# Kernel optimization log

Measured on AMD Instinct MI355X. Metric: run time of the kernel, lower is better.

The kernel has to match this reference:

```python
import jax, jax.numpy as jnp
import numpy as np

B, L, D = 2, 1024, 768
N_LAYERS, D_STATE, D_CONV, EXPAND = 4, 16, 4, 2
D_INNER = EXPAND * D
DT_RANK = (D + 15) // 16  # 48, ceil(d_model/16) as in reference Mamba
N_CLS = 10
EPS = 1e-6


def rmsnorm(x, w):
    return x * jax.lax.rsqrt(jnp.mean(x * x, axis=-1, keepdims=True) + EPS) * w


def mamba_block(x, in_w, conv_w, conv_b, xp_w, dt_w, dt_b, A_log, D_skip, out_w):
    # x: (B, L, D)
    Bsz = x.shape[0]
    xz = jnp.einsum('bld,ed->ble', x, in_w)            # (B, L, 2*d_inner)
    xi, z = jnp.split(xz, 2, axis=-1)
    # causal depthwise conv over the sequence dim
    xc = jnp.transpose(xi, (0, 2, 1))                  # (B, d_inner, L)
    xc = jax.lax.conv_general_dilated(
        xc, conv_w[:, None, :], (1,), [(D_CONV - 1, 0)],
        dimension_numbers=('NCH', 'OIH', 'NCH'), feature_group_count=D_INNER)
    xc = jnp.transpose(xc, (0, 2, 1)) + conv_b         # (B, L, d_inner)
    xc = jax.nn.silu(xc)
    # input-dependent SSM parameters
    x_dbl = jnp.einsum('bld,ed->ble', xc, xp_w)        # (B, L, dt_rank + 2*d_state)
    dt, Bs, Cs = jnp.split(x_dbl, [DT_RANK, DT_RANK + D_STATE], axis=-1)
    delta = jax.nn.softplus(jnp.einsum('blr,dr->bld', dt, dt_w) + dt_b)  # (B, L, d_inner)
    A = -jnp.exp(A_log)                                # (d_inner, d_state)
    dA = jnp.exp(delta[..., None] * A)                 # (B, L, d_inner, d_state)
    dBu = delta[..., None] * Bs[:, :, None, :] * xc[..., None]

    def step(h, inp):
        dA_t, dBu_t, C_t = inp
        h = dA_t * h + dBu_t                           # (B, d_inner, d_state)
        y = jnp.einsum('bdn,bn->bd', h, C_t)
        return h, y

    h0 = jnp.zeros((Bsz, D_INNER, D_STATE), x.dtype)
    _, ys = jax.lax.scan(step, h0, (jnp.swapaxes(dA, 0, 1),
                                    jnp.swapaxes(dBu, 0, 1),
                                    jnp.swapaxes(Cs, 0, 1)))
    y = jnp.swapaxes(ys, 0, 1) + xc * D_skip           # (B, L, d_inner)
    y = y * jax.nn.silu(z)                             # gate
    return jnp.einsum('bld,od->blo', y, out_w)


def reference(x, norm_w, in_proj_w, conv_w, conv_b, x_proj_w, dt_proj_w, dt_proj_b,
              A_log, D_skip, out_proj_w, final_norm_w,
              head1_w, head1_b, head_norm_w, head2_w, head2_b):
    for i in range(N_LAYERS):
        res = x
        x = rmsnorm(x, norm_w[i])
        x = mamba_block(x, in_proj_w[i], conv_w[i], conv_b[i], x_proj_w[i],
                        dt_proj_w[i], dt_proj_b[i], A_log[i], D_skip[i],
                        out_proj_w[i]) + res
    x = rmsnorm(x, final_norm_w)
    last = x[:, -1, :]                                 # (B, D)
    h = last @ head1_w.T + head1_b
    h = rmsnorm(h, head_norm_w)
    h = jax.nn.gelu(h, approximate=False)              # torch nn.GELU default is exact erf
    return h @ head2_w.T + head2_b                     # (B, N_CLS)


def setup_inputs() -> dict:
    key = jax.random.key(0)
    ks = jax.random.split(key, 10)
    s = 0.02
    x = jax.random.normal(ks[0], (B, L, D), jnp.float32)
    norm_w = jnp.ones((N_LAYERS, D), jnp.float32)
    in_proj_w = s * jax.random.normal(ks[1], (N_LAYERS, 2 * D_INNER, D), jnp.float32)
    conv_w = s * jax.random.normal(ks[2], (N_LAYERS, D_INNER, D_CONV), jnp.float32)
    conv_b = jnp.zeros((N_LAYERS, D_INNER), jnp.float32)
    x_proj_w = s * jax.random.normal(ks[3], (N_LAYERS, DT_RANK + 2 * D_STATE, D_INNER), jnp.float32)
    dt_proj_w = s * jax.random.normal(ks[4], (N_LAYERS, D_INNER, DT_RANK), jnp.float32)
    dt_proj_b = jnp.full((N_LAYERS, D_INNER), -4.6, jnp.float32)  # softplus(-4.6) ~ 0.01
    A_log = jnp.log(jnp.broadcast_to(
        jnp.arange(1, D_STATE + 1, dtype=jnp.float32), (N_LAYERS, D_INNER, D_STATE)) + 0.0)
    D_skip = jnp.ones((N_LAYERS, D_INNER), jnp.float32)
    out_proj_w = s * jax.random.normal(ks[5], (N_LAYERS, D, D_INNER), jnp.float32)
    final_norm_w = jnp.ones((D,), jnp.float32)
    head1_w = s * jax.random.normal(ks[6], (D, D), jnp.float32)
    head1_b = jnp.zeros((D,), jnp.float32)
    head_norm_w = jnp.ones((D,), jnp.float32)
    head2_w = s * jax.random.normal(ks[7], (N_CLS, D), jnp.float32)
    head2_b = jnp.zeros((N_CLS,), jnp.float32)
    return {"x": x, "norm_w": norm_w, "in_proj_w": in_proj_w, "conv_w": conv_w,
            "conv_b": conv_b, "x_proj_w": x_proj_w, "dt_proj_w": dt_proj_w,
            "dt_proj_b": dt_proj_b, "A_log": A_log, "D_skip": D_skip,
            "out_proj_w": out_proj_w, "final_norm_w": final_norm_w,
            "head1_w": head1_w, "head1_b": head1_b, "head_norm_w": head_norm_w,
            "head2_w": head2_w, "head2_b": head2_b}
```

## Files before the change

kernel.cpp:

```cpp
#include <hip/hip_runtime.h>
#include <hip/hip_bf16.h>
#include <math.h>

typedef __bf16 bf16;
typedef __bf16 bf16x4 __attribute__((ext_vector_type(4)));
typedef __bf16 bf16x8 __attribute__((ext_vector_type(8)));
typedef float floatx4 __attribute__((ext_vector_type(4)));

#define BB 2
#define LL 1024
#define DD 768
#define DI 1536
#define MROWS 2048
#define NXP 80
#define DTRANK 48
#define DTPAD 64
#define DSTATE 16
#define NC 16
#define CLEN 64
#define KSPLIT 16
#define OPKS 4
#define LOG2E 1.4426950408889634f
#define TROW 132
#define SYROW 68

__device__ __forceinline__ void ld16(void* lds, const void* g) {
    __builtin_amdgcn_global_load_lds(
        (const __attribute__((address_space(1))) void*)g,
        (__attribute__((address_space(3))) void*)lds, 16, 0, 0);
}

__device__ __forceinline__ void wait_vm0() {
    asm volatile("s_waitcnt vmcnt(0)" ::: "memory");
}

__device__ __forceinline__ float row16_sum(float x) {
    float t;
    t = __int_as_float(__builtin_amdgcn_update_dpp(0, __float_as_int(x), 0x111, 0xF, 0xF, true)); x += t;
    t = __int_as_float(__builtin_amdgcn_update_dpp(0, __float_as_int(x), 0x112, 0xF, 0xF, true)); x += t;
    t = __int_as_float(__builtin_amdgcn_update_dpp(0, __float_as_int(x), 0x114, 0xF, 0xF, true)); x += t;
    t = __int_as_float(__builtin_amdgcn_update_dpp(0, __float_as_int(x), 0x118, 0xF, 0xF, true)); x += t;
    return x;
}

__device__ __forceinline__ float exp2_raw(float x) {
#if __has_builtin(__builtin_amdgcn_exp2f)
    return __builtin_amdgcn_exp2f(x);
#else
    float r; asm("v_exp_f32 %0, %1" : "=v"(r) : "v"(x)); return r;
#endif
}

#define N1 (4 * 3072 * 768)
#define N2 (4 * NXP * DI)
#define N3 (4 * DI * DTPAD)
#define N4 (4 * DD * DI)
__global__ __launch_bounds__(256) void cvt_all_k(const float* __restrict__ in_proj_w,
                                                 const float* __restrict__ x_proj_w,
                                                 const float* __restrict__ dt_proj_w,
                                                 const float* __restrict__ out_proj_w,
                                                 bf16* __restrict__ w_in,
                                                 bf16* __restrict__ w_xp,
                                                 bf16* __restrict__ w_dt,
                                                 bf16* __restrict__ w_out) {
    int i = blockIdx.x * 256 + threadIdx.x;
    if (i < N1) { w_in[i] = (bf16)in_proj_w[i]; return; }
    i -= N1;
    if (i < N2) { w_xp[i] = (bf16)x_proj_w[i]; return; }
    i -= N2;
    if (i < N3) {
        int row = i >> 6, c = i & 63;
        w_dt[i] = (c < DTRANK) ? (bf16)dt_proj_w[row * DTRANK + c] : (bf16)0.f;
        return;
    }
    i -= N3;
    if (i < N4) w_out[i] = (bf16)out_proj_w[i];
}

__global__ __launch_bounds__(256) void rmsnorm_k(const float* __restrict__ x,
                                                 const float* __restrict__ w,
                                                 bf16* __restrict__ out) {
    int row = blockIdx.x;
    const float* xr = x + (size_t)row * DD;
    int tid = threadIdx.x;
    float v[3]; float ss = 0.f;
    for (int j = 0; j < 3; j++) { v[j] = xr[tid + j * 256]; ss += v[j] * v[j]; }
    for (int o = 1; o < 64; o <<= 1) ss += __shfl_xor(ss, o, 64);
    __shared__ float sred[4];
    if ((tid & 63) == 0) sred[tid >> 6] = ss;
    __syncthreads();
    float scale = rsqrtf((sred[0] + sred[1] + sred[2] + sred[3]) / (float)DD + 1e-6f);
    for (int j = 0; j < 3; j++) {
        int c = tid + j * 256;
        out[(size_t)row * DD + c] = (bf16)(v[j] * scale * w[c]);
    }
}

template <int MODE>
__global__ __launch_bounds__(256) void gemm_bt(const bf16* __restrict__ A,
                                               const bf16* __restrict__ W,
                                               float* __restrict__ Cf,
                                               bf16* __restrict__ Cb,
                                               int M, int N, int K) {
    __shared__ bf16 As[128][32];
    __shared__ bf16 Ws[128][32];
    const int tid  = threadIdx.x;
    const int m0   = blockIdx.x * 128;
    const int n0   = blockIdx.y * 128;
    const int wave = tid >> 6;
    const int lane = tid & 63;
    const int wm   = (wave >> 1) * 64;
    const int wn   = (wave & 1) * 64;
    const int lrow = lane & 15;
    const int quad = lane >> 4;

    int kbeg = 0, kend = K;
    if constexpr (MODE == 5) {
        int kseg = K / gridDim.z;
        kbeg = blockIdx.z * kseg;
        kend = kbeg + kseg;
        Cf  += (size_t)blockIdx.z * M * N;
    }

    floatx4 acc[4][4];
    for (int mi = 0; mi < 4; mi++)
        for (int ni = 0; ni < 4; ni++) acc[mi][ni] = (floatx4){0.f, 0.f, 0.f, 0.f};

    const int r0  = tid >> 2;
    const int r1  = r0 + 64;
    const int seg = (tid & 3) * 8;
    char* asb0 = (char*)As + wave * 1024;
    char* asb1 = (char*)As + 4096 + wave * 1024;
    char* wsb0 = (char*)Ws + wave * 1024;
    char* wsb1 = (char*)Ws + 4096 + wave * 1024;

    for (int kb = kbeg; kb < kend; kb += 32) {
        int gk = kb + seg;
        __syncthreads();
        ld16(asb0, A + (size_t)(m0 + r0) * K + gk);
        ld16(asb1, A + (size_t)(m0 + r1) * K + gk);
        ld16(wsb0, W + (size_t)(n0 + r0) * K + gk);
        ld16(wsb1, W + (size_t)(n0 + r1) * K + gk);
        wait_vm0();
        __syncthreads();
        bf16x8 af[4], wf[4];
        for (int mi = 0; mi < 4; mi++) af[mi] = *(const bf16x8*)&As[wm + mi * 16 + lrow][quad * 8];
        for (int ni = 0; ni < 4; ni++) wf[ni] = *(const bf16x8*)&Ws[wn + ni * 16 + lrow][quad * 8];
        for (int mi = 0; mi < 4; mi++)
            for (int ni = 0; ni < 4; ni++)
                acc[mi][ni] = __builtin_amdgcn_mfma_f32_16x16x32_bf16(af[mi], wf[ni], acc[mi][ni], 0, 0, 0);
    }
    for (int mi = 0; mi < 4; mi++) {
        int rowb = m0 + wm + mi * 16 + quad * 4;
        for (int ni = 0; ni < 4; ni++) {
            int col = n0 + wn + ni * 16 + lrow;
            for (int r = 0; r < 4; r++) {
                int row = rowb + r;
                float v = acc[mi][ni][r];
                if constexpr (MODE == 1) Cb[(size_t)row * N + col] = (bf16)v;
                else                     Cf[(size_t)row * N + col] = v;
            }
        }
    }
}

__global__ __launch_bounds__(256) void op_reduce_norm_k(const float* __restrict__ part,
                                                        const float* __restrict__ resid,
                                                        const float* __restrict__ nw,
                                                        float* __restrict__ xout,
                                                        bf16* __restrict__ xnb) {
    int row = blockIdx.x;
    int tid = threadIdx.x;
    float v[3]; float ss = 0.f;
    for (int j = 0; j < 3; j++) {
        int c = tid + j * 256;
        size_t idx = (size_t)row * DD + c;
        float s = resid[idx];
        for (int ks = 0; ks < OPKS; ks++) s += part[(size_t)ks * MROWS * DD + idx];
        v[j] = s;
        xout[idx] = s;
        ss += s * s;
    }
    for (int o = 1; o < 64; o <<= 1) ss += __shfl_xor(ss, o, 64);
    __shared__ float sred[4];
    if ((tid & 63) == 0) sred[tid >> 6] = ss;
    __syncthreads();
    float scale = rsqrtf((sred[0] + sred[1] + sred[2] + sred[3]) / (float)DD + 1e-6f);
    for (int j = 0; j < 3; j++) {
        int c = tid + j * 256;
        xnb[(size_t)row * DD + c] = (bf16)(v[j] * scale * nw[c]);
    }
}

__global__ __launch_bounds__(256) void gemm_xp(const bf16* __restrict__ A,
                                               const bf16* __restrict__ W,
                                               float* __restrict__ part) {
    __shared__ bf16 As[64][40];
    __shared__ bf16 Ws[128][40];
    const int tid  = threadIdx.x;
    const int m0   = blockIdx.x * 64;
    const int ks   = blockIdx.y;
    const int k0   = ks * (DI / KSPLIT);
    const int wave = tid >> 6;
    const int lane = tid & 63;
    const int lrow = lane & 15;
    const int quad = lane >> 4;
    const int wm   = wave * 16;

    floatx4 acc[5];
    for (int ni = 0; ni < 5; ni++) acc[ni] = (floatx4){0.f, 0.f, 0.f, 0.f};

    const int ra  = tid >> 2;
    const int rw1 = ra + 64;
    const int seg = (tid & 3) * 8;

    for (int kb = 0; kb < DI / KSPLIT; kb += 32) {
        int gk = k0 + kb + seg;
        bf16x8 va = *(const bf16x8*)(A + (size_t)(m0 + ra) * DI + gk);
        bf16x8 vw0, vw1;
        if (ra < NXP) vw0 = *(const bf16x8*)(W + (size_t)ra * DI + gk);
        else          for (int j = 0; j < 8; j++) vw0[j] = (bf16)0.f;
        if (rw1 < NXP) vw1 = *(const bf16x8*)(W + (size_t)rw1 * DI + gk);
        else           for (int j = 0; j < 8; j++) vw1[j] = (bf16)0.f;
        __syncthreads();
        *(bf16x8*)&As[ra][seg]  = va;
        *(bf16x8*)&Ws[ra][seg]  = vw0;
        *(bf16x8*)&Ws[rw1][seg] = vw1;
        __syncthreads();
        bf16x8 af = *(const bf16x8*)&As[wm + lrow][quad * 8];
        for (int ni = 0; ni < 5; ni++) {
            bf16x8 wf = *(const bf16x8*)&Ws[ni * 16 + lrow][quad * 8];
            acc[ni] = __builtin_amdgcn_mfma_f32_16x16x32_bf16(af, wf, acc[ni], 0, 0, 0);
        }
    }
    float* pout = part + (size_t)ks * MROWS * NXP;
    for (int ni = 0; ni < 5; ni++) {
        int col = ni * 16 + lrow;
        for (int r = 0; r < 4; r++) {
            int row = m0 + wm + quad * 4 + r;
            pout[(size_t)row * NXP + col] = acc[ni][r];
        }
    }
}

__global__ __launch_bounds__(256) void xp_reduce_k(const float* __restrict__ part,
                                                   float* __restrict__ xdbl,
                                                   bf16* __restrict__ dtbf) {
    int idx = blockIdx.x * 256 + threadIdx.x;
    if (idx >= MROWS * NXP) return;
    float s = 0.f;
    for (int j = 0; j < KSPLIT; j++) s += part[(size_t)j * MROWS * NXP + idx];
    xdbl[idx] = s;
    int m = idx / NXP, c = idx - m * NXP;
    if (c < DTRANK)      dtbf[m * DTPAD + c] = (bf16)s;
    else if (c < DTPAD)  dtbf[m * DTPAD + c] = (bf16)0.f;
}

__global__ __launch_bounds__(256) void conv_silu_k(const bf16* __restrict__ xz,
                                                   const float* __restrict__ cw,
                                                   const float* __restrict__ cb,
                                                   bf16* __restrict__ xcb,
                                                   bf16* __restrict__ gzb) {
    int t = blockIdx.x * 256 + threadIdx.x;
    if (t >= MROWS * (DI / 4)) return;
    int m = t / (DI / 4);
    int d = (t - m * (DI / 4)) * 4;
    int l = m & (LL - 1);
    float acc[4];
    floatx4 cwv[4];
    for (int q = 0; q < 4; q++) {
        acc[q] = cb[d + q];
        cwv[q] = *(const floatx4*)&cw[(d + q) * 4];
    }
    for (int k = 0; k < 4; k++) {
        int lp = l - 3 + k;
        if (lp >= 0) {
            bf16x4 v = *(const bf16x4*)&xz[(size_t)(m - 3 + k) * (2 * DI) + d];
            for (int q = 0; q < 4; q++) acc[q] += (float)v[q] * cwv[q][k];
        }
    }
    bf16x4 xo, go;
    bf16x4 z4 = *(const bf16x4*)&xz[(size_t)m * (2 * DI) + DI + d];
    for (int q = 0; q < 4; q++) {
        float s = acc[q] / (1.f + __expf(-acc[q]));
        xo[q] = (bf16)s;
        float zv = (float)z4[q];
        go[q] = (bf16)(zv / (1.f + __expf(-zv)));
    }
    *(bf16x4*)&xcb[(size_t)m * DI + d] = xo;
    *(bf16x4*)&gzb[(size_t)m * DI + d] = go;
}

__global__ __launch_bounds__(256) void scan1_k(const bf16* __restrict__ dtb,
                                               const bf16* __restrict__ wdt,
                                               const float* __restrict__ dtbias,
                                               const bf16* __restrict__ xcb,
                                               const float* __restrict__ xdbl,
                                               const float* __restrict__ A_log,
                                               float* __restrict__ Pbuf,
                                               float* __restrict__ Sbuf) {
    const int b   = blockIdx.y;
    const int d0  = blockIdx.x * 16;
    const int c   = blockIdx.z;
    const int tid = threadIdx.x;
    const int dl  = tid >> 4;
    const int n   = tid & 15;
    const int wv  = tid >> 6;
    const int lane = tid & 63;
    const int lr  = lane & 15;
    const int q   = lane >> 4;
    const int l0  = c * CLEN;

    const float a2 = -__expf(A_log[(size_t)(d0 + dl) * DSTATE + n]) * LOG2E;
    const float bi = dtbias[d0 + lr];

    __shared__ __align__(16) bf16  Bdt[16][72];
    __shared__ __align__(16) bf16  Adt[CLEN][64];
    __shared__ __align__(16) float sbraw[CLEN][16];
    __shared__ __align__(16) bf16  sxc[CLEN][16];
    __shared__ __align__(16) float sdpT[16][TROW];
    __shared__ __align__(16) float sbT[16][68];

    {
        int s = tid, row = s >> 3, cc = s & 7;
        ld16((char*)&Adt[0][0] + (s & ~63) * 16,
             dtb + (size_t)(b * LL + l0 + row) * DTPAD + ((cc ^ (row & 7)) << 3));
        s = tid + 256; row = s >> 3; cc = s & 7;
        ld16((char*)&Adt[0][0] + (s & ~63) * 16,
             dtb + (size_t)(b * LL + l0 + row) * DTPAD + ((cc ^ (row & 7)) << 3));
        {
            int r2 = tid >> 2, c2 = tid & 3;
            ld16((char*)&sbraw[0][0] + (tid & ~63) * 16,
                 xdbl + (size_t)(b * LL + l0 + r2) * NXP + DTRANK + c2 * 4);
        }
        if (tid < 128) {
            int r2 = tid >> 1, c2 = tid & 1;
            ld16((char*)&sxc[0][0] + (tid & ~63) * 16,
                 xcb + (size_t)(b * LL + l0 + r2) * DI + d0 + c2 * 8);
            int r = tid >> 3, s2 = (tid & 7) * 8;
            *(bf16x8*)&Bdt[r][s2] = *(const bf16x8*)&wdt[(size_t)(d0 + r) * DTPAD + s2];
        }
    }
    wait_vm0();
    __syncthreads();

    {
        floatx4 dacc = (floatx4){0.f, 0.f, 0.f, 0.f};
        const char* arow = (const char*)&Adt[16 * wv + lr][0];
        bf16x8 a0 = *(const bf16x8*)(arow + ((q ^ (lr & 7)) << 4));
        bf16x8 a1 = *(const bf16x8*)(arow + (((4 + q) ^ (lr & 7)) << 4));
        dacc = __builtin_amdgcn_mfma_f32_16x16x32_bf16(
            a0, *(const bf16x8*)&Bdt[lr][q * 8], dacc, 0, 0, 0);
        dacc = __builtin_amdgcn_mfma_f32_16x16x32_bf16(
            a1, *(const bf16x8*)&Bdt[lr][32 + q * 8], dacc, 0, 0, 0);
        float vv[4], xvv[4];
        #pragma unroll
        for (int r = 0; r < 4; ++r) {
            int l = 16 * wv + q * 4 + r;
            float v = dacc[r] + bi;
            v = (v > 20.f) ? v : log1pf(__expf(v));
            vv[r] = v; xvv[r] = (float)sxc[l][lr];
        }
        int L0 = 16 * wv + q * 4;
        *(float4*)&sdpT[lr][2 * L0] =
            make_float4(vv[0], vv[0] * xvv[0], vv[1], vv[1] * xvv[1]);
        *(float4*)&sdpT[lr][2 * L0 + 4] =
            make_float4(vv[2], vv[2] * xvv[2], vv[3], vv[3] * xvv[3]);
        #pragma unroll
        for (int k2 = 0; k2 < 4; ++k2) {
            int idx = tid + 256 * k2, ii = idx >> 4, dd2 = idx & 15;
            sbT[dd2][ii] = sbraw[ii][dd2];
        }
    }
    __syncthreads();

    float h = 0.f, sd = 0.f;
    {
        const float4* dpr = (const float4*)&sdpT[dl][0];
        const float4* bpr = (const float4*)&sbT[n][0];
        float4 dA[4], dB2[4], bA[2], bB2[2];
        #pragma unroll
        for (int t = 0; t < 4; ++t) dA[t] = dpr[t];
        #pragma unroll
        for (int t = 0; t < 2; ++t) bA[t] = bpr[t];
        #pragma unroll
        for (int g = 0; g < 8; ++g) {
            if (g + 1 < 8) {
                #pragma unroll
                for (int t = 0; t < 4; ++t) {
                    if ((g & 1) == 0) dB2[t] = dpr[(g + 1) * 4 + t];
                    else              dA[t]  = dpr[(g + 1) * 4 + t];
                }
                #pragma unroll
                for (int t = 0; t < 2; ++t) {
                    if ((g & 1) == 0) bB2[t] = bpr[(g + 1) * 2 + t];
                    else              bA[t]  = bpr[(g + 1) * 2 + t];
                }
            }
            #pragma unroll
            for (int i = 0; i < 8; ++i) {
                float4 v = ((g & 1) == 0) ? dA[i >> 1] : dB2[i >> 1];
                float4 w = ((g & 1) == 0) ? bA[i >> 2] : bB2[i >> 2];
                float dvx = (i & 1) ? v.z : v.x;
                float dpy = (i & 1) ? v.w : v.y;
                float bx  = ((i & 3) == 0) ? w.x : ((i & 3) == 1) ? w.y
                          : ((i & 3) == 2) ? w.z : w.w;
                float e = exp2_raw(dvx * a2);
                h = __builtin_fmaf(e, h, dpy * bx);
                sd += dvx;
            }
        }
    }
    size_t o = (((size_t)c * BB + b) * DI + (d0 + dl)) * DSTATE + n;
    Pbuf[o] = exp2_raw(a2 * sd);
    Sbuf[o] = h;
}

__global__ __launch_bounds__(256) void compose_k(const float* __restrict__ P,
                                                 const float* __restrict__ S,
                                                 float* __restrict__ H0) {
    int idx = blockIdx.x * 256 + threadIdx.x;
    const size_t stride = (size_t)BB * DI * DSTATE;
    float h = 0.f;
    #pragma unroll
    for (int c = 0; c < NC; ++c) {
        H0[(size_t)c * stride + idx] = h;
        h = __builtin_fmaf(P[(size_t)c * stride + idx], h, S[(size_t)c * stride + idx]);
    }
}

__global__ __launch_bounds__(256) void scan2_k(const bf16* __restrict__ dtb,
                                               const bf16* __restrict__ wdt,
                                               const float* __restrict__ dtbias,
                                               const bf16* __restrict__ xcb,
                                               const bf16* __restrict__ gzb,
                                               const float* __restrict__ xdbl,
                                               const float* __restrict__ A_log,
                                               const float* __restrict__ Dskip,
                                               const float* __restrict__ H0buf,
                                               bf16* __restrict__ ybf) {
    const int b   = blockIdx.y;
    const int d0  = blockIdx.x * 16;
    const int c   = blockIdx.z;
    const int tid = threadIdx.x;
    const int dl  = tid >> 4;
    const int n   = tid & 15;
    const int wv  = tid >> 6;
    const int lane = tid & 63;
    const int lr  = lane & 15;
    const int q   = lane >> 4;
    const int l0  = c * CLEN;

    const float a2 = -__expf(A_log[(size_t)(d0 + dl) * DSTATE + n]) * LOG2E;
    const float bi = dtbias[d0 + lr];

    __shared__ __align__(16) bf16  Bdt[16][72];
    __shared__ __align__(16) bf16  sxc[CLEN][16];
    __shared__ __align__(16) bf16  sgz[CLEN][16];
    __shared__ __align__(16) float sdpT[16][TROW];
    __shared__ __align__(16) float sbcT[16][TROW];
    __shared__ __align__(16) char  sov[16384];
    bf16  (*Adt)[64]     = (bf16 (*)[64])sov;
    float (*sbcraw)[32]  = (float (*)[32])(sov + 8192);
    float (*syT)[SYROW]  = (float (*)[SYROW])sov;

    float h = H0buf[((size_t)c * BB + b) * (DI * DSTATE) + (size_t)(d0 + dl) * DSTATE + n];

    {
        int s = tid, row = s >> 3, cc = s & 7;
        ld16((char*)&Adt[0][0] + (s & ~63) * 16,
             dtb + (size_t)(b * LL + l0 + row) * DTPAD + ((cc ^ (row & 7)) << 3));
        ld16((char*)&sbcraw[0][0] + (s & ~63) * 16,
             xdbl + (size_t)(b * LL + l0 + row) * NXP + DTRANK + cc * 4);
        s = tid + 256; row = s >> 3; cc = s & 7;
        ld16((char*)&Adt[0][0] + (s & ~63) * 16,
             dtb + (size_t)(b * LL + l0 + row) * DTPAD + ((cc ^ (row & 7)) << 3));
        ld16((char*)&sbcraw[0][0] + (s & ~63) * 16,
             xdbl + (size_t)(b * LL + l0 + row) * NXP + DTRANK + cc * 4);
        if (tid < 128) {
            int r2 = tid >> 1, c2 = tid & 1;
            ld16((char*)&sxc[0][0] + (tid & ~63) * 16,
                 xcb + (size_t)(b * LL + l0 + r2) * DI + d0 + c2 * 8);
            int r = tid >> 3, s2 = (tid & 7) * 8;
            *(bf16x8*)&Bdt[r][s2] = *(const bf16x8*)&wdt[(size_t)(d0 + r) * DTPAD + s2];
        } else {
            int t2 = tid - 128, r2 = t2 >> 1, c2 = t2 & 1;
            ld16((char*)&sgz[0][0] + (t2 & ~63) * 16,
                 gzb + (size_t)(b * LL + l0 + r2) * DI + d0 + c2 * 8);
        }
    }
    wait_vm0();
    __syncthreads();

    {
        floatx4 dacc = (floatx4){0.f, 0.f, 0.f, 0.f};
        const char* arow = (const char*)&Adt[16 * wv + lr][0];
        bf16x8 a0 = *(const bf16x8*)(arow + ((q ^ (lr & 7)) << 4));
        bf16x8 a1 = *(const bf16x8*)(arow + (((4 + q) ^ (lr & 7)) << 4));
        dacc = __builtin_amdgcn_mfma_f32_16x16x32_bf16(
            a0, *(const bf16x8*)&Bdt[lr][q * 8], dacc, 0, 0, 0);
        dacc = __builtin_amdgcn_mfma_f32_16x16x32_bf16(
            a1, *(const bf16x8*)&Bdt[lr][32 + q * 8], dacc, 0, 0, 0);
        float vv[4], xvv[4];
        #pragma unroll
        for (int r = 0; r < 4; ++r) {
            int l = 16 * wv + q * 4 + r;
            float v = dacc[r] + bi;
            v = (v > 20.f) ? v : log1pf(__expf(v));
            vv[r] = v; xvv[r] = (float)sxc[l][lr];
        }
        int L0 = 16 * wv + q * 4;
        *(float4*)&sdpT[lr][2 * L0] =
            make_float4(vv[0], vv[0] * xvv[0], vv[1], vv[1] * xvv[1]);
        *(float4*)&sdpT[lr][2 * L0 + 4] =
            make_float4(vv[2], vv[2] * xvv[2], vv[3], vv[3] * xvv[3]);
        #pragma unroll
        for (int k2 = 0; k2 < 4; ++k2) {
            int idx = tid + 256 * k2, ii = idx >> 4, dd2 = idx & 15;
            *(float2*)&sbcT[dd2][2 * ii] =
                make_float2(sbcraw[ii][dd2], sbcraw[ii][16 + dd2]);
        }
    }
    __syncthreads();

    {
        const float4* dpr = (const float4*)&sdpT[dl][0];
        const float4* bcr = (const float4*)&sbcT[n][0];
        float4 dA[4], bA[4], dB2[4], bB2[4];
        float y4[4];
        #pragma unroll
        for (int t = 0; t < 4; ++t) { dA[t] = dpr[t]; bA[t] = bcr[t]; }
        #pragma unroll
        for (int g = 0; g < 8; ++g) {
            #pragma unroll
            for (int t = 0; t < 4; ++t) {
                if (g + 1 < 8) {
                    if ((g & 1) == 0) { dB2[t] = dpr[(g + 1) * 4 + t]; bB2[t] = bcr[(g + 1) * 4 + t]; }
                    else              { dA[t]  = dpr[(g + 1) * 4 + t]; bA[t]  = bcr[(g + 1) * 4 + t]; }
                }
            }
            #pragma unroll
            for (int i = 0; i < 8; ++i) {
                float4 v = ((g & 1) == 0) ? dA[i >> 1] : dB2[i >> 1];
                float4 w = ((g & 1) == 0) ? bA[i >> 1] : bB2[i >> 1];
                float dvx = (i & 1) ? v.z : v.x;
                float dpy = (i & 1) ? v.w : v.y;
                float bx  = (i & 1) ? w.z : w.x;
                float cy  = (i & 1) ? w.w : w.y;
                float e = exp2_raw(dvx * a2);
                h = __builtin_fmaf(e, h, dpy * bx);
                y4[i & 3] = row16_sum(h * cy);
                if ((i & 3) == 3 && n == 0) {
                    *(floatx4*)&syT[dl][g * 8 + i - 3] =
                        (floatx4){y4[0], y4[1], y4[2], y4[3]};
                }
            }
        }
    }
    __syncthreads();

    #pragma unroll
    for (int k2 = 0; k2 < 4; ++k2) {
        int idx = tid + 256 * k2, ii = idx >> 4, dd = idx & 15;
        float xv = (float)sxc[ii][dd];
        float gv = (float)sgz[ii][dd];
        float yv = (syT[dd][ii] + xv * Dskip[d0 + dd]) * gv;
        ybf[(size_t)(b * LL + l0 + ii) * DI + d0 + dd] = (bf16)yv;
    }
}

__global__ __launch_bounds__(256) void head_norm_k(const float* __restrict__ x,
                                                   const float* __restrict__ fnw,
                                                   float* __restrict__ xn_buf) {
    int b = blockIdx.x;
    int tid = threadIdx.x;
    const float* xr = x + ((size_t)b * LL + (LL - 1)) * DD;
    __shared__ float sred[4];
    float v[3]; float ss = 0.f;
    for (int j = 0; j < 3; j++) { v[j] = xr[tid + j * 256]; ss += v[j] * v[j]; }
    for (int o = 1; o < 64; o <<= 1) ss += __shfl_xor(ss, o, 64);
    if ((tid & 63) == 0) sred[tid >> 6] = ss;
    __syncthreads();
    float scale = rsqrtf((sred[0] + sred[1] + sred[2] + sred[3]) / (float)DD + 1e-6f);
    for (int j = 0; j < 3; j++) {
        int c = tid + j * 256;
        xn_buf[(size_t)b * DD + c] = v[j] * scale * fnw[c];
    }
}

__global__ __launch_bounds__(256) void head_h1_k(const float* __restrict__ xn_buf,
                                                 const float* __restrict__ h1w,
                                                 const float* __restrict__ h1b,
                                                 float* __restrict__ h_buf) {
    int b  = blockIdx.x;
    int o0 = blockIdx.y * 64;
    int tid = threadIdx.x;
    __shared__ float sx[DD];
    for (int c = tid; c < DD; c += 256) sx[c] = xn_buf[(size_t)b * DD + c];
    __syncthreads();
    int wave = tid >> 6, lane = tid & 63;
    for (int j = 0; j < 16; j++) {
        int o = o0 + wave * 16 + j;
        const float* wrow = h1w + (size_t)o * DD;
        float acc = 0.f;
        for (int k = 0; k < 12; k++) {
            int c = lane + 64 * k;
            acc += wrow[c] * sx[c];
        }
        for (int off = 1; off < 64; off <<= 1) acc += __shfl_xor(acc, off, 64);
        if (lane == 0) h_buf[(size_t)b * DD + o] = acc + h1b[o];
    }
}

__global__ __launch_bounds__(256) void head_out_k(const float* __restrict__ h_buf,
                                                  const float* __restrict__ hnw,
                                                  const float* __restrict__ h2w,
                                                  const float* __restrict__ h2b,
                                                  float* __restrict__ out) {
    int b = blockIdx.x;
    int tid = threadIdx.x;
    __shared__ float hh[DD];
    __shared__ float sred[4];
    const float* hr = h_buf + (size_t)b * DD;
    float ss = 0.f;
    for (int c = tid; c < DD; c += 256) { float v = hr[c]; ss += v * v; }
    for (int o = 1; o < 64; o <<= 1) ss += __shfl_xor(ss, o, 64);
    if ((tid & 63) == 0) sred[tid >> 6] = ss;
    __syncthreads();
    float sc = rsqrtf((sred[0] + sred[1] + sred[2] + sred[3]) / (float)DD + 1e-6f);
    for (int c = tid; c < DD; c += 256) {
        float v = hr[c] * sc * hnw[c];
        hh[c] = 0.5f * v * (1.f + erff(v * 0.70710678118f));
    }
    __syncthreads();
    int w = tid >> 6, lane = tid & 63;
    for (int j = w; j < 10; j += 4) {
        float acc = 0.f;
        const float* wrow = h2w + (size_t)j * DD;
        for (int c = lane; c < DD; c += 64) acc += hh[c] * wrow[c];
        for (int o = 1; o < 64; o <<= 1) acc += __shfl_xor(acc, o, 64);
        if (lane == 0) out[b * 10 + j] = acc + h2b[j];
    }
}

extern "C" void kernel_launch(void* const* d_in, const int* in_sizes, int n_in,
                              void* d_out, int out_size, void* d_ws, size_t ws_size,
                              hipStream_t stream) {
    const float* x_in      = (const float*)d_in[0];
    const float* norm_w    = (const float*)d_in[1];
    const float* in_proj_w = (const float*)d_in[2];
    const float* conv_w    = (const float*)d_in[3];
    const float* conv_b    = (const float*)d_in[4];
    const float* x_proj_w  = (const float*)d_in[5];
    const float* dt_proj_w = (const float*)d_in[6];
    const float* dt_proj_b = (const float*)d_in[7];
    const float* A_log     = (const float*)d_in[8];
    const float* D_skip    = (const float*)d_in[9];
    const float* out_proj_w= (const float*)d_in[10];
    const float* fnw       = (const float*)d_in[11];
    const float* h1w       = (const float*)d_in[12];
    const float* h1b       = (const float*)d_in[13];
    const float* hnw       = (const float*)d_in[14];
    const float* h2w       = (const float*)d_in[15];
    const float* h2b       = (const float*)d_in[16];
    float* out = (float*)d_out;

    char* ws = (char*)d_ws;
    size_t off = 0;
    auto alloc = [&](size_t bytes) -> void* {
        void* p = ws + off;
        off += (bytes + 255) & ~(size_t)255;
        return p;
    };
    bf16* w_in  = (bf16*)alloc((size_t)N1 * 2);
    bf16* w_xp  = (bf16*)alloc((size_t)N2 * 2);
    bf16* w_dt  = (bf16*)alloc((size_t)N3 * 2);
    bf16* w_out = (bf16*)alloc((size_t)N4 * 2);
    bf16* xn_bf = (bf16*)alloc((size_t)MROWS * DD * 2);
    bf16* xz_bf = (bf16*)alloc((size_t)MROWS * 2 * DI * 2);
    bf16* xc_bf = (bf16*)alloc((size_t)MROWS * DI * 2);
    bf16* gz_bf = (bf16*)alloc((size_t)MROWS * DI * 2);
    float* xdbl = (float*)alloc((size_t)MROWS * NXP * 4);
    bf16* dt_bf = (bf16*)alloc((size_t)MROWS * DTPAD * 2);
    bf16* y_bf  = (bf16*)alloc((size_t)MROWS * DI * 2);
    float* x_buf= (float*)alloc((size_t)MROWS * DD * 4);
    float* Pbuf = (float*)alloc((size_t)NC * BB * DI * DSTATE * 4);
    float* Sbuf = (float*)alloc((size_t)NC * BB * DI * DSTATE * 4);
    float* H0buf= (float*)alloc((size_t)NC * BB * DI * DSTATE * 4);
    float* xnl  = (float*)alloc((size_t)BB * DD * 4);
    float* hbuf = (float*)alloc((size_t)BB * DD * 4);
    float* xp_part = (float*)alloc((size_t)KSPLIT * MROWS * NXP * 4);
    float* op_part = (float*)alloc((size_t)OPKS * MROWS * DD * 4);

    {
        int ntot = N1 + N2 + N3 + N4;
        cvt_all_k<<<(ntot + 255) / 256, 256, 0, stream>>>(
            in_proj_w, x_proj_w, dt_proj_w, out_proj_w, w_in, w_xp, w_dt, w_out);
    }

    for (int i = 0; i < 4; i++) {
        const float* x_src = (i == 0) ? x_in : x_buf;
        if (i == 0)
            rmsnorm_k<<<MROWS, 256, 0, stream>>>(x_src, norm_w, xn_bf);
        gemm_bt<1><<<dim3(MROWS / 128, 3072 / 128), 256, 0, stream>>>(
            xn_bf, w_in + (size_t)i * 3072 * 768, nullptr, xz_bf,
            MROWS, 2 * DI, DD);
        conv_silu_k<<<(MROWS * (DI / 4) + 255) / 256, 256, 0, stream>>>(
            xz_bf, conv_w + (size_t)i * DI * 4, conv_b + (size_t)i * DI, xc_bf, gz_bf);
        gemm_xp<<<dim3(MROWS / 64, KSPLIT), 256, 0, stream>>>(
            xc_bf, w_xp + (size_t)i * NXP * DI, xp_part);
        xp_reduce_k<<<(MROWS * NXP + 255) / 256, 256, 0, stream>>>(xp_part, xdbl, dt_bf);
        scan1_k<<<dim3(DI / 16, BB, NC), 256, 0, stream>>>(
            dt_bf, w_dt + (size_t)i * DI * DTPAD, dt_proj_b + (size_t)i * DI,
            xc_bf, xdbl, A_log + (size_t)i * DI * DSTATE, Pbuf, Sbuf);
        compose_k<<<(BB * DI * DSTATE) / 256, 256, 0, stream>>>(Pbuf, Sbuf, H0buf);
        scan2_k<<<dim3(DI / 16, BB, NC), 256, 0, stream>>>(
            dt_bf, w_dt + (size_t)i * DI * DTPAD, dt_proj_b + (size_t)i * DI,
            xc_bf, gz_bf, xdbl, A_log + (size_t)i * DI * DSTATE,
            D_skip + (size_t)i * DI, H0buf, y_bf);
        gemm_bt<5><<<dim3(MROWS / 128, DD / 128, OPKS), 256, 0, stream>>>(
            y_bf, w_out + (size_t)i * DD * DI, op_part, nullptr,
            MROWS, DD, DI);
        op_reduce_norm_k<<<MROWS, 256, 0, stream>>>(
            op_part, x_src, norm_w + ((i + 1) & 3) * DD, x_buf, xn_bf);
    }

    head_norm_k<<<BB, 256, 0, stream>>>(x_buf, fnw, xnl);
    head_h1_k<<<dim3(BB, DD / 64), 256, 0, stream>>>(xnl, h1w, h1b, hbuf);
    head_out_k<<<BB, 256, 0, stream>>>(hbuf, hnw, h2w, h2b, out);
}
```

Baseline: 658.5 us.

## Process two chunks per scan block with register prefetch of next chunk

```diff
diff --git a/kernel.cpp b/kernel.cpp
--- a/kernel.cpp
+++ b/kernel.cpp
@@ -301,7 +301,7 @@
                                                float* __restrict__ Sbuf) {
     const int b   = blockIdx.y;
     const int d0  = blockIdx.x * 16;
-    const int c   = blockIdx.z;
+    const int c0  = blockIdx.z * 2;
     const int tid = threadIdx.x;
     const int dl  = tid >> 4;
     const int n   = tid & 15;
@@ -309,50 +309,40 @@
     const int lane = tid & 63;
     const int lr  = lane & 15;
     const int q   = lane >> 4;
-    const int l0  = c * CLEN;
 
     const float a2 = -__expf(A_log[(size_t)(d0 + dl) * DSTATE + n]) * LOG2E;
     const float bi = dtbias[d0 + lr];
 
-    __shared__ __align__(16) bf16  Bdt[16][72];
-    __shared__ __align__(16) bf16  Adt[CLEN][64];
-    __shared__ __align__(16) float sbraw[CLEN][16];
     __shared__ __align__(16) bf16  sxc[CLEN][16];
     __shared__ __align__(16) float sdpT[16][TROW];
     __shared__ __align__(16) float sbT[16][68];
 
-    {
-        int s = tid, row = s >> 3, cc = s & 7;
-        ld16((char*)&Adt[0][0] + (s & ~63) * 16,
-             dtb + (size_t)(b * LL + l0 + row) * DTPAD + ((cc ^ (row & 7)) << 3));
-        s = tid + 256; row = s >> 3; cc = s & 7;
-        ld16((char*)&Adt[0][0] + (s & ~63) * 16,
-             dtb + (size_t)(b * LL + l0 + row) * DTPAD + ((cc ^ (row & 7)) << 3));
-        {
-            int r2 = tid >> 2, c2 = tid & 3;
-            ld16((char*)&sbraw[0][0] + (tid & ~63) * 16,
-                 xdbl + (size_t)(b * LL + l0 + r2) * NXP + DTRANK + c2 * 4);
-        }
+    const bf16x8 wf0 = *(const bf16x8*)&wdt[(size_t)(d0 + lr) * DTPAD + q * 8];
+    const bf16x8 wf1 = *(const bf16x8*)&wdt[(size_t)(d0 + lr) * DTPAD + 32 + q * 8];
+
+    auto ldA = [&](int l0, bf16x8& a0, bf16x8& a1) {
+        const bf16* r = &dtb[(size_t)(b * LL + l0 + 16 * wv + lr) * DTPAD + q * 8];
+        a0 = *(const bf16x8*)r;
+        a1 = *(const bf16x8*)(r + 32);
+    };
+    auto ldB = [&](int l0, float* Bv) {
+        #pragma unroll
+        for (int k2 = 0; k2 < 4; ++k2) {
+            int ii = (tid + 256 * k2) >> 4;
+            Bv[k2] = xdbl[(size_t)(b * LL + l0 + ii) * NXP + DTRANK + n];
+        }
+    };
+    auto dma_x = [&](int l0) {
         if (tid < 128) {
             int r2 = tid >> 1, c2 = tid & 1;
             ld16((char*)&sxc[0][0] + (tid & ~63) * 16,
                  xcb + (size_t)(b * LL + l0 + r2) * DI + d0 + c2 * 8);
-            int r = tid >> 3, s2 = (tid & 7) * 8;
-            *(bf16x8*)&Bdt[r][s2] = *(const bf16x8*)&wdt[(size_t)(d0 + r) * DTPAD + s2];
-        }
-    }
-    wait_vm0();
-    __syncthreads();
-
-    {
+        }
+    };
+    auto pack = [&](bf16x8 a0, bf16x8 a1, const float* Bv) {
         floatx4 dacc = (floatx4){0.f, 0.f, 0.f, 0.f};
-        const char* arow = (const char*)&Adt[16 * wv + lr][0];
-        bf16x8 a0 = *(const bf16x8*)(arow + ((q ^ (lr & 7)) << 4));
-        bf16x8 a1 = *(const bf16x8*)(arow + (((4 + q) ^ (lr & 7)) << 4));
-        dacc = __builtin_amdgcn_mfma_f32_16x16x32_bf16(
-            a0, *(const bf16x8*)&Bdt[lr][q * 8], dacc, 0, 0, 0);
-        dacc = __builtin_amdgcn_mfma_f32_16x16x32_bf16(
-            a1, *(const bf16x8*)&Bdt[lr][32 + q * 8], dacc, 0, 0, 0);
+        dacc = __builtin_amdgcn_mfma_f32_16x16x32_bf16(a0, wf0, dacc, 0, 0, 0);
+        dacc = __builtin_amdgcn_mfma_f32_16x16x32_bf16(a1, wf1, dacc, 0, 0, 0);
         float vv[4], xvv[4];
         #pragma unroll
         for (int r = 0; r < 4; ++r) {
@@ -368,14 +358,12 @@
             make_float4(vv[2], vv[2] * xvv[2], vv[3], vv[3] * xvv[3]);
         #pragma unroll
         for (int k2 = 0; k2 < 4; ++k2) {
-            int idx = tid + 256 * k2, ii = idx >> 4, dd2 = idx & 15;
-            sbT[dd2][ii] = sbraw[ii][dd2];
-        }
-    }
-    __syncthreads();
-
-    float h = 0.f, sd = 0.f;
-    {
+            int ii = (tid + 256 * k2) >> 4;
+            sbT[n][ii] = Bv[k2];
+        }
+    };
+    auto scanloc = [&](int c) {
+        float h = 0.f, sd = 0.f;
         const float4* dpr = (const float4*)&sdpT[dl][0];
         const float4* bpr = (const float4*)&sbT[n][0];
         float4 dA[4], dB2[4], bA[2], bB2[2];
@@ -410,10 +398,33 @@
                 sd += dvx;
             }
         }
-    }
-    size_t o = (((size_t)c * BB + b) * DI + (d0 + dl)) * DSTATE + n;
-    Pbuf[o] = exp2_raw(a2 * sd);
-    Sbuf[o] = h;
+        size_t o = (((size_t)c * BB + b) * DI + (d0 + dl)) * DSTATE + n;
+        Pbuf[o] = exp2_raw(a2 * sd);
+        Sbuf[o] = h;
+    };
+
+    const int l0 = c0 * CLEN;
+    bf16x8 a0, a1, a0n, a1n;
+    float Bv[4], Bvn[4];
+
+    ldA(l0, a0, a1);
+    ldB(l0, Bv);
+    dma_x(l0);
+    wait_vm0();
+    __syncthreads();
+
+    pack(a0, a1, Bv);
+    __syncthreads();
+    ldA(l0 + CLEN, a0n, a1n);
+    ldB(l0 + CLEN, Bvn);
+    dma_x(l0 + CLEN);
+    scanloc(c0);
+    wait_vm0();
+    __syncthreads();
+
+    pack(a0n, a1n, Bvn);
+    __syncthreads();
+    scanloc(c0 + 1);
 }
 
 __global__ __launch_bounds__(256) void compose_k(const float* __restrict__ P,
@@ -441,7 +452,7 @@
                                                bf16* __restrict__ ybf) {
     const int b   = blockIdx.y;
     const int d0  = blockIdx.x * 16;
-    const int c   = blockIdx.z;
+    const int c0  = blockIdx.z * 2;
     const int tid = threadIdx.x;
     const int dl  = tid >> 4;
     const int n   = tid & 15;
@@ -449,58 +460,50 @@
     const int lane = tid & 63;
     const int lr  = lane & 15;
     const int q   = lane >> 4;
-    const int l0  = c * CLEN;
-
-    const float a2 = -__expf(A_log[(size_t)(d0 + dl) * DSTATE + n]) * LOG2E;
-    const float bi = dtbias[d0 + lr];
-
-    __shared__ __align__(16) bf16  Bdt[16][72];
-    __shared__ __align__(16) bf16  sxc[CLEN][16];
-    __shared__ __align__(16) bf16  sgz[CLEN][16];
-    __shared__ __align__(16) float sdpT[16][TROW];
-    __shared__ __align__(16) float sbcT[16][TROW];
-    __shared__ __align__(16) char  sov[16384];
-    bf16  (*Adt)[64]     = (bf16 (*)[64])sov;
-    float (*sbcraw)[32]  = (float (*)[32])(sov + 8192);
-    float (*syT)[SYROW]  = (float (*)[SYROW])sov;
-
-    float h = H0buf[((size_t)c * BB + b) * (DI * DSTATE) + (size_t)(d0 + dl) * DSTATE + n];
-
-    {
-        int s = tid, row = s >> 3, cc = s & 7;
-        ld16((char*)&Adt[0][0] + (s & ~63) * 16,
-             dtb + (size_t)(b * LL + l0 + row) * DTPAD + ((cc ^ (row & 7)) << 3));
-        ld16((char*)&sbcraw[0][0] + (s & ~63) * 16,
-             xdbl + (size_t)(b * LL + l0 + row) * NXP + DTRANK + cc * 4);
-        s = tid + 256; row = s >> 3; cc = s & 7;
-        ld16((char*)&Adt[0][0] + (s & ~63) * 16,
-             dtb + (size_t)(b * LL + l0 + row) * DTPAD + ((cc ^ (row & 7)) << 3));
-        ld16((char*)&sbcraw[0][0] + (s & ~63) * 16,
-             xdbl + (size_t)(b * LL + l0 + row) * NXP + DTRANK + cc * 4);
+
+    const float a2  = -__expf(A_log[(size_t)(d0 + dl) * DSTATE + n]) * LOG2E;
+    const float bi  = dtbias[d0 + lr];
+    const float dsk = Dskip[d0 + lr];
+
+    __shared__ __align__(16) bf16   sxc[CLEN][16];
+    __shared__ __align__(16) bf16   sgz[CLEN][16];
+    __shared__ __align__(16) float  sdpT[16][TROW];
+    __shared__ __align__(16) float  sbcT[16][TROW];
+    __shared__ __align__(16) float2 ssk[CLEN][16];
+    __shared__ __align__(16) float  syT[16][SYROW];
+
+    const bf16x8 wf0 = *(const bf16x8*)&wdt[(size_t)(d0 + lr) * DTPAD + q * 8];
+    const bf16x8 wf1 = *(const bf16x8*)&wdt[(size_t)(d0 + lr) * DTPAD + 32 + q * 8];
+
+    auto ldA = [&](int l0, bf16x8& a0, bf16x8& a1) {
+        const bf16* r = &dtb[(size_t)(b * LL + l0 + 16 * wv + lr) * DTPAD + q * 8];
+        a0 = *(const bf16x8*)r;
+        a1 = *(const bf16x8*)(r + 32);
+    };
+    auto ldBC = [&](int l0, float* Bv, float* Cv) {
+        #pragma unroll
+        for (int k2 = 0; k2 < 4; ++k2) {
+            int ii = (tid + 256 * k2) >> 4;
+            const float* p = &xdbl[(size_t)(b * LL + l0 + ii) * NXP + DTRANK + n];
+            Bv[k2] = p[0];
+            Cv[k2] = p[DSTATE];
+        }
+    };
+    auto dma_xg = [&](int l0) {
         if (tid < 128) {
             int r2 = tid >> 1, c2 = tid & 1;
             ld16((char*)&sxc[0][0] + (tid & ~63) * 16,
                  xcb + (size_t)(b * LL + l0 + r2) * DI + d0 + c2 * 8);
-            int r = tid >> 3, s2 = (tid & 7) * 8;
-            *(bf16x8*)&Bdt[r][s2] = *(const bf16x8*)&wdt[(size_t)(d0 + r) * DTPAD + s2];
         } else {
             int t2 = tid - 128, r2 = t2 >> 1, c2 = t2 & 1;
             ld16((char*)&sgz[0][0] + (t2 & ~63) * 16,
                  gzb + (size_t)(b * LL + l0 + r2) * DI + d0 + c2 * 8);
         }
-    }
-    wait_vm0();
-    __syncthreads();
-
-    {
+    };
+    auto pack = [&](bf16x8 a0, bf16x8 a1, const float* Bv, const float* Cv) {
         floatx4 dacc = (floatx4){0.f, 0.f, 0.f, 0.f};
-        const char* arow = (const char*)&Adt[16 * wv + lr][0];
-        bf16x8 a0 = *(const bf16x8*)(arow + ((q ^ (lr & 7)) << 4));
-        bf16x8 a1 = *(const bf16x8*)(arow + (((4 + q) ^ (lr & 7)) << 4));
-        dacc = __builtin_amdgcn_mfma_f32_16x16x32_bf16(
-            a0, *(const bf16x8*)&Bdt[lr][q * 8], dacc, 0, 0, 0);
-        dacc = __builtin_amdgcn_mfma_f32_16x16x32_bf16(
-            a1, *(const bf16x8*)&Bdt[lr][32 + q * 8], dacc, 0, 0, 0);
+        dacc = __builtin_amdgcn_mfma_f32_16x16x32_bf16(a0, wf0, dacc, 0, 0, 0);
+        dacc = __builtin_amdgcn_mfma_f32_16x16x32_bf16(a1, wf1, dacc, 0, 0, 0);
         float vv[4], xvv[4];
         #pragma unroll
         for (int r = 0; r < 4; ++r) {
@@ -508,6 +511,8 @@
             float v = dacc[r] + bi;
             v = (v > 20.f) ? v : log1pf(__expf(v));
             vv[r] = v; xvv[r] = (float)sxc[l][lr];
+            float gv = (float)sgz[l][lr];
+            ssk[l][lr] = make_float2(xvv[r] * dsk, gv);
         }
         int L0 = 16 * wv + q * 4;
         *(float4*)&sdpT[lr][2 * L0] =
@@ -516,14 +521,11 @@
             make_float4(vv[2], vv[2] * xvv[2], vv[3], vv[3] * xvv[3]);
         #pragma unroll
         for (int k2 = 0; k2 < 4; ++k2) {
-            int idx = tid + 256 * k2, ii = idx >> 4, dd2 = idx & 15;
-            *(float2*)&sbcT[dd2][2 * ii] =
-                make_float2(sbcraw[ii][dd2], sbcraw[ii][16 + dd2]);
-        }
-    }
-    __syncthreads();
-
-    {
+            int ii = (tid + 256 * k2) >> 4;
+            *(float2*)&sbcT[n][2 * ii] = make_float2(Bv[k2], Cv[k2]);
+        }
+    };
+    auto scan64 = [&](float& h) {
         const float4* dpr = (const float4*)&sdpT[dl][0];
         const float4* bcr = (const float4*)&sbcT[n][0];
         float4 dA[4], bA[4], dB2[4], bB2[4];
@@ -556,17 +558,45 @@
                 }
             }
         }
-    }
-    __syncthreads();
-
-    #pragma unroll
-    for (int k2 = 0; k2 < 4; ++k2) {
-        int idx = tid + 256 * k2, ii = idx >> 4, dd = idx & 15;
-        float xv = (float)sxc[ii][dd];
-        float gv = (float)sgz[ii][dd];
-        float yv = (syT[dd][ii] + xv * Dskip[d0 + dd]) * gv;
-        ybf[(size_t)(b * LL + l0 + ii) * DI + d0 + dd] = (bf16)yv;
-    }
+    };
+    auto emit = [&](int l0) {
+        #pragma unroll
+        for (int k2 = 0; k2 < 4; ++k2) {
+            int idx = tid + 256 * k2, ii = idx >> 4, dd = idx & 15;
+            float2 sk = ssk[ii][dd];
+            float yv = (syT[dd][ii] + sk.x) * sk.y;
+            ybf[(size_t)(b * LL + l0 + ii) * DI + d0 + dd] = (bf16)yv;
+        }
+    };
+
+    const int l0 = c0 * CLEN;
+    float h = H0buf[((size_t)c0 * BB + b) * (DI * DSTATE) + (size_t)(d0 + dl) * DSTATE + n];
+
+    bf16x8 a0, a1, a0n, a1n;
+    float Bv[4], Cv[4], Bvn[4], Cvn[4];
+
+    ldA(l0, a0, a1);
+    ldBC(l0, Bv, Cv);
+    dma_xg(l0);
+    wait_vm0();
+    __syncthreads();
+
+    pack(a0, a1, Bv, Cv);
+    __syncthreads();
+    ldA(l0 + CLEN, a0n, a1n);
+    ldBC(l0 + CLEN, Bvn, Cvn);
+    dma_xg(l0 + CLEN);
+    scan64(h);
+    __syncthreads();
+    wait_vm0();
+    emit(l0);
+    __syncthreads();
+
+    pack(a0n, a1n, Bvn, Cvn);
+    __syncthreads();
+    scan64(h);
+    __syncthreads();
+    emit(l0 + CLEN);
 }
 
 __global__ __launch_bounds__(256) void head_norm_k(const float* __restrict__ x,
@@ -710,11 +740,11 @@
         gemm_xp<<<dim3(MROWS / 64, KSPLIT), 256, 0, stream>>>(
             xc_bf, w_xp + (size_t)i * NXP * DI, xp_part);
         xp_reduce_k<<<(MROWS * NXP + 255) / 256, 256, 0, stream>>>(xp_part, xdbl, dt_bf);
-        scan1_k<<<dim3(DI / 16, BB, NC), 256, 0, stream>>>(
+        scan1_k<<<dim3(DI / 16, BB, NC / 2), 256, 0, stream>>>(
             dt_bf, w_dt + (size_t)i * DI * DTPAD, dt_proj_b + (size_t)i * DI,
             xc_bf, xdbl, A_log + (size_t)i * DI * DSTATE, Pbuf, Sbuf);
         compose_k<<<(BB * DI * DSTATE) / 256, 256, 0, stream>>>(Pbuf, Sbuf, H0buf);
-        scan2_k<<<dim3(DI / 16, BB, NC), 256, 0, stream>>>(
+        scan2_k<<<dim3(DI / 16, BB, NC / 2), 256, 0, stream>>>(
             dt_bf, w_dt + (size_t)i * DI * DTPAD, dt_proj_b + (size_t)i * DI,
             xc_bf, gz_bf, xdbl, A_log + (size_t)i * DI * DSTATE,
             D_skip + (size_t)i * DI, H0buf, y_bf);
```

New measurement: 670.8 us. Within noise of the previous version (+1.9%).
